# Optimization experiments

Hardware: AMD Instinct MI355X
Metric: run time of the kernel (lower is better)

Reference implementation:

```python
import jax, jax.numpy as jnp
import numpy as np

B, N, K = 8, 4096, 20
C_IN, H = 4, 64
EPS = 1e-5


def _bn(h, g, b):
    # BatchNorm1d in training mode: stats over all leading dims, per channel
    axes = tuple(range(h.ndim - 1))
    m = jnp.mean(h, axis=axes, keepdims=True)
    v = jnp.var(h, axis=axes, keepdims=True)
    return (h - m) * jax.lax.rsqrt(v + EPS) * g + b


def _edgeconv(x, k, w1, b1, g1, be1, w2, b2, g2, be2):
    # x: [B, N, C]. Dynamic kNN graph on current features (per cloud).
    x2 = jnp.sum(x * x, axis=-1)                       # [B, N]
    d = x2[:, :, None] + x2[:, None, :] - 2.0 * jnp.einsum('bnc,bmc->bnm', x, x)
    d = jax.lax.stop_gradient(d)                        # knn indices are non-differentiable
    _, idx = jax.lax.top_k(-d, k)                       # [B, N, k] nearest (incl. self)
    x_j = jax.vmap(lambda xb, ib: xb[ib])(x, idx)       # [B, N, k, C] gather
    x_i = jnp.broadcast_to(x[:, :, None, :], x_j.shape)
    msg = jnp.concatenate([x_i, x_j - x_i], axis=-1)    # [B, N, k, 2C]
    h = jax.nn.relu(_bn(msg @ w1 + b1, g1, be1))
    h = jax.nn.relu(_bn(h @ w2 + b2, g2, be2))
    return jnp.max(h, axis=2)                           # max aggregation over neighbors


def _forward(x,
             c1_w1, c1_b1, c1_g1, c1_be1, c1_w2, c1_b2, c1_g2, c1_be2,
             c2_w1, c2_b1, c2_g1, c2_be1, c2_w2, c2_b2, c2_g2, c2_be2,
             cls_w1, cls_b1, cls_g1, cls_be1, cls_w2, cls_b2):
    x1 = _edgeconv(x, K, c1_w1, c1_b1, c1_g1, c1_be1, c1_w2, c1_b2, c1_g2, c1_be2)   # [B,N,64]
    x2 = _edgeconv(x1, K, c2_w1, c2_b1, c2_g1, c2_be1, c2_w2, c2_b2, c2_g2, c2_be2)  # [B,N,128]
    xc = jnp.concatenate([x1, x2], axis=-1).reshape(B * N, 3 * H)                    # [BN,192]
    h = jax.nn.relu(_bn(xc @ cls_w1 + cls_b1, cls_g1, cls_be1))                      # dropout=identity (eval)
    return h @ cls_w2 + cls_b2                                                       # [BN, 1]


def setup_inputs() -> dict:
    key = jax.random.key(0)
    ks = iter(jax.random.split(key, 24))
    lin = lambda k, di, do: jax.random.normal(k, (di, do), jnp.float32) / np.sqrt(di)
    inp = {'x': jax.random.normal(next(ks), (B, N, C_IN), jnp.float32)}
    # conv1 nn: Linear(8,64)->BN->ReLU->Linear(64,64)->BN->ReLU
    inp.update(c1_w1=lin(next(ks), 2 * C_IN, H), c1_b1=jnp.zeros(H), c1_g1=jnp.ones(H), c1_be1=jnp.zeros(H),
               c1_w2=lin(next(ks), H, H), c1_b2=jnp.zeros(H), c1_g2=jnp.ones(H), c1_be2=jnp.zeros(H))
    # conv2 nn: Linear(128,128)->BN->ReLU->Linear(128,128)->BN->ReLU
    H2 = 2 * H
    inp.update(c2_w1=lin(next(ks), H2, H2), c2_b1=jnp.zeros(H2), c2_g1=jnp.ones(H2), c2_be1=jnp.zeros(H2),
               c2_w2=lin(next(ks), H2, H2), c2_b2=jnp.zeros(H2), c2_g2=jnp.ones(H2), c2_be2=jnp.zeros(H2))
    # classifier: Linear(192,128)->BN->ReLU->Dropout->Linear(128,1)
    inp.update(cls_w1=lin(next(ks), 3 * H, 128), cls_b1=jnp.zeros(128), cls_g1=jnp.ones(128), cls_be1=jnp.zeros(128),
               cls_w2=lin(next(ks), 128, 1), cls_b2=jnp.zeros(1))
    return inp


def reference(x,
              c1_w1, c1_b1, c1_g1, c1_be1, c1_w2, c1_b2, c1_g2, c1_be2,
              c2_w1, c2_b1, c2_g1, c2_be1, c2_w2, c2_b2, c2_g2, c2_be2,
              cls_w1, cls_b1, cls_g1, cls_be1, cls_w2, cls_b2):
    return _forward(x,
                    c1_w1, c1_b1, c1_g1, c1_be1, c1_w2, c1_b2, c1_g2, c1_be2,
                    c2_w1, c2_b1, c2_g1, c2_be1, c2_w2, c2_b2, c2_g2, c2_be2,
                    cls_w1, cls_b1, cls_g1, cls_be1, cls_w2, cls_b2)
```

## Files before the change

### kernel.cpp

```cpp
#include <hip/hip_runtime.h>
#include <math.h>

#define B_ 8
#define N_ 4096
#define K_ 20
#define KS_ 24
#define BN_ (B_*N_)

typedef __attribute__((ext_vector_type(8))) short bf16x8;
typedef __attribute__((ext_vector_type(4))) float f32x4;

__global__ __launch_bounds__(256) void finalize_parts_kernel(
    const double* __restrict__ part, int nb, int H, double invCount, float* __restrict__ st)
{
    __shared__ double red[256], red2[256];
    const int c = blockIdx.x, t = threadIdx.x;
    double s = 0., s2 = 0.;
    for (int b = t; b < nb; b += 256) {
        s  += part[(size_t)b*2*H + c];
        s2 += part[(size_t)b*2*H + H + c];
    }
    red[t] = s; red2[t] = s2;
    __syncthreads();
    #pragma unroll
    for (int off = 128; off; off >>= 1) {
        if (t < off) { red[t] += red[t+off]; red2[t] += red2[t+off]; }
        __syncthreads();
    }
    if (t == 0) {
        double mean = red[0] * invCount;
        double var  = fmax(red2[0] * invCount - mean * mean, 0.);
        st[2*H + c] = (float)mean;
        st[3*H + c] = (float)(1.0 / sqrt(var + 1e-5));
    }
}

__global__ __launch_bounds__(1024, 8) void knn4_kernel(const float* __restrict__ x, int* __restrict__ idxout)
{
    __shared__ float4 xt[N_];
    const int b = blockIdx.y;
    const int t = threadIdx.x;
    const float4* xg = (const float4*)x + b*N_;
    for (int e = t; e < N_; e += 1024) xt[e] = xg[e];
    __syncthreads();
    const int w = t >> 6, L = t & 63;
    const int n = blockIdx.x*16 + w;
    const float4 q = xt[n];
    const float MX = 3.4e38f;
    float m1 = MX, m2 = MX, m3 = MX; int i1 = 0, i2 = 0, i3 = 0;
    #pragma unroll 1
    for (int j = 0; j < 64; ++j) {
        float4 vv = xt[(j<<6) | L];
        float nn = vv.x*vv.x + vv.y*vv.y + vv.z*vv.z + vv.w*vv.w;
        float dp = q.x*vv.x + q.y*vv.y + q.z*vv.z + q.w*vv.w;
        float v = nn - 2.f*dp;
        bool c1 = v < m1, c2 = v < m2, c3 = v < m3;
        m3 = c2 ? m2 : (c3 ? v : m3);
        i3 = c2 ? i2 : (c3 ? j : i3);
        m2 = c1 ? m1 : (c2 ? v : m2);
        i2 = c1 ? i1 : (c2 ? j : i2);
        m1 = c1 ? v : m1;
        i1 = c1 ? j : i1;
    }
    unsigned long long used = 0;
    int mywin = 0;
    #pragma unroll 1
    for (int r = 0; r < K_; ++r) {
        float bv = m1; int bg = (i1<<6) | L;
        #pragma unroll
        for (int off = 32; off; off >>= 1) {
            float ov = __shfl_xor(bv, off);
            int   og = __shfl_xor(bg, off);
            bool tk = (ov < bv) || (ov == bv && og < bg);
            bv = tk ? ov : bv; bg = tk ? og : bg;
        }
        if (L == r) mywin = bg;
        if (L == (bg & 63)) {
            used |= 1ull << i1;
            m1 = m2; i1 = i2; m2 = m3; i2 = i3; m3 = MX;
            if (m1 == MX) {
                m2 = MX; m3 = MX; i1 = 0; i2 = 0; i3 = 0;
                #pragma unroll 1
                for (int j = 0; j < 64; ++j) {
                    float4 vv = xt[(j<<6) | L];
                    float nn = vv.x*vv.x + vv.y*vv.y + vv.z*vv.z + vv.w*vv.w;
                    float dp = q.x*vv.x + q.y*vv.y + q.z*vv.z + q.w*vv.w;
                    float dj = nn - 2.f*dp;
                    float v = ((used >> j) & 1ull) ? MX : dj;
                    bool c1 = v < m1, c2 = v < m2, c3 = v < m3;
                    m3 = c2 ? m2 : (c3 ? v : m3);
                    i3 = c2 ? i2 : (c3 ? j : i3);
                    m2 = c1 ? m1 : (c2 ? v : m2);
                    i2 = c1 ? i1 : (c2 ? j : i2);
                    m1 = c1 ? v : m1;
                    i1 = c1 ? j : i1;
                }
            }
        }
    }
    if (L < K_) idxout[(b*N_ + n)*K_ + L] = mywin;
}

static __device__ inline unsigned short f2bf(float f)
{
    unsigned u = __float_as_uint(f);
    unsigned r = (u + 0x7fffu + ((u >> 16) & 1u)) >> 16;
    return (unsigned short)r;
}

__global__ __launch_bounds__(256) void nrmprep_kernel(const float* __restrict__ x,
                                                      unsigned short* __restrict__ Xh,
                                                      unsigned short* __restrict__ Xl,
                                                      float* __restrict__ nrm)
{
    const int t = threadIdx.x, L = t & 63;
    const int row = blockIdx.x*4 + (t >> 6);
    const float v = x[row*64 + L];
    float s = v * v;
    #pragma unroll
    for (int off = 32; off; off >>= 1) s += __shfl_xor(s, off);
    if (L == 0) nrm[row] = s;
    unsigned short h = f2bf(v);
    float hf = __uint_as_float((unsigned)h << 16);
    unsigned short l = f2bf(v - hf);
    const size_t base = (size_t)(row >> 4)*1024 + (size_t)(L >> 3)*128 + (size_t)(row & 15)*8 + (size_t)(L & 7);
    Xh[base] = h;
    Xl[base] = l;
}

#define CE_(x,y) { float _t = fminf(x,y); y = fmaxf(x,y); x = _t; }
#define SORT8_(g0,g1,g2,g3,g4,g5,g6,g7)                                   \
    CE_(g0,g1) CE_(g2,g3) CE_(g4,g5) CE_(g6,g7)                           \
    CE_(g0,g2) CE_(g1,g3) CE_(g4,g6) CE_(g5,g7)                           \
    CE_(g1,g2) CE_(g5,g6)                                                 \
    CE_(g0,g4) CE_(g1,g5) CE_(g2,g6) CE_(g3,g7)                           \
    CE_(g2,g4) CE_(g3,g5)                                                 \
    CE_(g1,g2) CE_(g3,g4) CE_(g5,g6)
#define MERGE8_(g0,g1,g2,g3,g4,g5,g6,g7)                                  \
    sm0 = fminf(sm0,g7); sm1 = fminf(sm1,g6); sm2 = fminf(sm2,g5);        \
    sm3 = fminf(sm3,g4); sm4 = fminf(sm4,g3); sm5 = fminf(sm5,g2);        \
    sm6 = fminf(sm6,g1); sm7 = fminf(sm7,g0);                             \
    CE_(sm0,sm4) CE_(sm1,sm5) CE_(sm2,sm6) CE_(sm3,sm7)                   \
    CE_(sm0,sm2) CE_(sm1,sm3) CE_(sm4,sm6) CE_(sm5,sm7)                   \
    CE_(sm0,sm1) CE_(sm2,sm3) CE_(sm4,sm5) CE_(sm6,sm7)

__global__ __launch_bounds__(1024, 4) void knn64v4_kernel(
    const unsigned short* __restrict__ Xh, const unsigned short* __restrict__ Xl,
    const float* __restrict__ nrm, int* __restrict__ idx24)
{
    __shared__ float dist[16*512];
    const int b = blockIdx.y, t = threadIdx.x;
    const int w = t >> 6, L = t & 63;
    const int q0 = blockIdx.x * 16;
    const int m = L & 15, q4 = L >> 4;
    const size_t rowbase = (size_t)b * N_ * 64;
    const int swzW = q4 << 4;
    const int swzR = (w >> 2) << 4;
    const int fragoff = q4*128 + m*8;

    const unsigned short* aph = Xh + rowbase + (size_t)(q0 >> 4)*1024 + fragoff;
    const unsigned short* apl = Xl + rowbase + (size_t)(q0 >> 4)*1024 + fragoff;
    const bf16x8 a_h0 = *(const bf16x8*)(aph);
    const bf16x8 a_h1 = *(const bf16x8*)(aph + 512);
    const bf16x8 a_l0 = *(const bf16x8*)(apl);
    const bf16x8 a_l1 = *(const bf16x8*)(apl + 512);

    const float MX = 3.4e38f;
    float sm0 = MX, sm1 = MX, sm2 = MX, sm3 = MX, sm4 = MX, sm5 = MX, sm6 = MX, sm7 = MX;

    float* const wrow = dist + q4*2048;
    float* const rrow = dist + w*512 + (L ^ swzR);

    #pragma unroll 1
    for (int ck = 0; ck < 8; ++ck) {
        const unsigned slotW0 = (unsigned)(ck*8);
        const unsigned short* bp_h = Xh + rowbase + (size_t)(ck*32 + w*2)*1024 + fragoff;
        const unsigned short* bp_l = Xl + rowbase + (size_t)(ck*32 + w*2)*1024 + fragoff;
        const float* np = nrm + b*N_ + ck*512 + w*32 + m;
        int cm = w*32 + m;
        __syncthreads();
        #pragma unroll
        for (int tt = 0; tt < 2; ++tt) {
            bf16x8 b_h0 = *(const bf16x8*)(bp_h);
            bf16x8 b_h1 = *(const bf16x8*)(bp_h + 512);
            bf16x8 b_l0 = *(const bf16x8*)(bp_l);
            bf16x8 b_l1 = *(const bf16x8*)(bp_l + 512);
            f32x4 acc = {0.f, 0.f, 0.f, 0.f};
            acc = __builtin_amdgcn_mfma_f32_16x16x32_bf16(a_h0, b_h0, acc, 0, 0, 0);
            acc = __builtin_amdgcn_mfma_f32_16x16x32_bf16(a_h1, b_h1, acc, 0, 0, 0);
            acc = __builtin_amdgcn_mfma_f32_16x16x32_bf16(a_l0, b_h0, acc, 0, 0, 0);
            acc = __builtin_amdgcn_mfma_f32_16x16x32_bf16(a_l1, b_h1, acc, 0, 0, 0);
            acc = __builtin_amdgcn_mfma_f32_16x16x32_bf16(a_h0, b_l0, acc, 0, 0, 0);
            acc = __builtin_amdgcn_mfma_f32_16x16x32_bf16(a_h1, b_l1, acc, 0, 0, 0);
            const float nv = *np;
            const int colW = cm ^ swzW;
            const unsigned slotW = slotW0 + (unsigned)(cm >> 6);
            float* wp = wrow + colW;
            #pragma unroll
            for (int r = 0; r < 4; ++r) {
                float dv = nv - 2.f*acc[r];
                unsigned key = (__float_as_uint(dv) & ~63u) | slotW;
                wp[r*512] = __uint_as_float(key);
            }
            bp_h += 1024; bp_l += 1024; np += 16; cm += 16;
        }
        __syncthreads();
        {
            float g0 = rrow[0*64], g1 = rrow[1*64], g2 = rrow[2*64], g3 = rrow[3*64];
            float g4 = rrow[4*64], g5 = rrow[5*64], g6 = rrow[6*64], g7 = rrow[7*64];
            SORT8_(g0,g1,g2,g3,g4,g5,g6,g7)
            MERGE8_(g0,g1,g2,g3,g4,g5,g6,g7)
        }
    }

    int mywin = 0;
    #pragma unroll 1
    for (int sr = 0; sr < 3; ++sr) {
        float a0 = sm0, a1 = sm1, a2 = sm2, a3 = sm3, a4 = sm4, a5 = sm5, a6 = sm6, a7 = sm7;
        #pragma unroll
        for (int off = 32; off; off >>= 1) {
            float b0 = __shfl_xor(a0, off), b1 = __shfl_xor(a1, off);
            float b2 = __shfl_xor(a2, off), b3 = __shfl_xor(a3, off);
            float b4 = __shfl_xor(a4, off), b5 = __shfl_xor(a5, off);
            float b6 = __shfl_xor(a6, off), b7 = __shfl_xor(a7, off);
            float c0 = fminf(a0, b7), c1 = fminf(a1, b6), c2 = fminf(a2, b5), c3 = fminf(a3, b4);
            float c4 = fminf(a4, b3), c5 = fminf(a5, b2), c6 = fminf(a6, b1), c7 = fminf(a7, b0);
            float u;
            u = fminf(c0, c4); c4 = fmaxf(c0, c4); c0 = u;
            u = fminf(c1, c5); c5 = fmaxf(c1, c5); c1 = u;
            u = fminf(c2, c6); c6 = fmaxf(c2, c6); c2 = u;
            u = fminf(c3, c7); c7 = fmaxf(c3, c7); c3 = u;
            u = fminf(c0, c2); c2 = fmaxf(c0, c2); c0 = u;
            u = fminf(c1, c3); c3 = fmaxf(c1, c3); c1 = u;
            u = fminf(c4, c6); c6 = fmaxf(c4, c6); c4 = u;
            u = fminf(c5, c7); c7 = fmaxf(c5, c7); c5 = u;
            u = fminf(c0, c1); c1 = fmaxf(c0, c1); c0 = u;
            u = fminf(c2, c3); c3 = fmaxf(c2, c3); c2 = u;
            u = fminf(c4, c5); c5 = fmaxf(c4, c5); c4 = u;
            u = fminf(c6, c7); c7 = fmaxf(c6, c7); c6 = u;
            a0 = c0; a1 = c1; a2 = c2; a3 = c3; a4 = c4; a5 = c5; a6 = c6; a7 = c7;
        }
        #define POPW(AW, WIDX)                                                              \
        {                                                                                   \
            const unsigned long long bal = __ballot(sm0 == (AW));                           \
            const int owner = (int)__ffsll(bal) - 1;                                        \
            if (L == sr*8 + (WIDX))                                                         \
                mywin = (int)(((__float_as_uint(AW) & 63u) << 6) | (unsigned)owner);        \
            if (L == owner) {                                                               \
                sm0 = sm1; sm1 = sm2; sm2 = sm3; sm3 = sm4;                                 \
                sm4 = sm5; sm5 = sm6; sm6 = sm7; sm7 = MX;                                  \
            }                                                                               \
        }
        POPW(a0, 0) POPW(a1, 1) POPW(a2, 2) POPW(a3, 3)
        POPW(a4, 4) POPW(a5, 5) POPW(a6, 6) POPW(a7, 7)
        #undef POPW
    }
    if (L < KS_) idx24[((size_t)b*N_ + q0 + w)*KS_ + L] = mywin;
}

__global__ __launch_bounds__(256) void rescore_kernel(const float* __restrict__ x1, const float* __restrict__ nrm,
                                                      const int* __restrict__ idx24, int* __restrict__ idxout)
{
    const int t = threadIdx.x, w = t >> 6, L = t & 63;
    const int p = blockIdx.x*4 + w;
    const int bbase = p & ~(N_-1);
    const float MX = 3.4e38f;
    float dv = MX; int di = 0x7fffffff;
    if (L < KS_) {
        const int ci = idx24[(size_t)p*KS_ + L];
        const float4* qr = (const float4*)(x1 + (size_t)p*64);
        const float4* cr = (const float4*)(x1 + (size_t)(bbase + ci)*64);
        float dot = 0.f;
        #pragma unroll
        for (int i = 0; i < 16; ++i) {
            float4 a = qr[i], bx = cr[i];
            dot += a.x*bx.x + a.y*bx.y + a.z*bx.z + a.w*bx.w;
        }
        dv = __fsub_rn(__fadd_rn(nrm[p], nrm[bbase + ci]), 2.f*dot);
        di = ci;
    }
    int myfin = 0;
    #pragma unroll 1
    for (int r = 0; r < K_/2; ++r) {
        float v1 = dv; int g1 = di;
        float v2 = MX; int g2 = 0x7fffffff;
        #pragma unroll
        for (int off = 32; off; off >>= 1) {
            float ov1 = __shfl_xor(v1, off); int og1 = __shfl_xor(g1, off);
            float ov2 = __shfl_xor(v2, off); int og2 = __shfl_xor(g2, off);
            bool c1 = (ov1 < v1) || (ov1 == v1 && og1 < g1);
            float hv = c1 ? v1 : ov1; int hg = c1 ? g1 : og1;
            v1 = c1 ? ov1 : v1;       g1 = c1 ? og1 : g1;
            bool c2 = (ov2 < v2) || (ov2 == v2 && og2 < g2);
            float l2v = c2 ? ov2 : v2; int l2g = c2 ? og2 : g2;
            bool c3 = (l2v < hv) || (l2v == hv && l2g < hg);
            v2 = c3 ? l2v : hv;  g2 = c3 ? l2g : hg;
        }
        if (L == 2*r)   myfin = g1;
        if (L == 2*r+1) myfin = g2;
        if (di == g1 || di == g2) dv = MX;
    }
    if (L < K_) idxout[(size_t)p*K_ + L] = myfin;
}

__global__ __launch_bounds__(256) void pq1_kernel(const float* __restrict__ x, const float* __restrict__ W,
                                                  const float* __restrict__ b1,
                                                  float* __restrict__ P, float* __restrict__ Q)
{
    __shared__ float wd[256], wb[256];
    const int t = threadIdx.x;
    wd[t] = W[t] - W[256 + t];
    wb[t] = W[256 + t];
    __syncthreads();
    const int p = blockIdx.x*4 + (t >> 6), c = t & 63;
    const float4 xv = ((const float4*)x)[p];
    float Pv = b1[c] + xv.x*wd[c] + xv.y*wd[64+c] + xv.z*wd[128+c] + xv.w*wd[192+c];
    float Qv =         xv.x*wb[c] + xv.y*wb[64+c] + xv.z*wb[128+c] + xv.w*wb[192+c];
    P[p*64 + c] = Pv;
    Q[p*64 + c] = Qv;
}

__global__ __launch_bounds__(256) void pq2_kernel(const float* __restrict__ x1, const float* __restrict__ W,
                                                  const float* __restrict__ b1,
                                                  float* __restrict__ P, float* __restrict__ Q)
{
    __shared__ float wd[64*128], wb[64*128];
    const int t = threadIdx.x;
    for (int e = t; e < 8192; e += 256) {
        float wt = W[e], wbo = W[8192 + e];
        wd[e] = wt - wbo; wb[e] = wbo;
    }
    __syncthreads();
    const int pl = t >> 7, c = t & 127;
    const float b1v = b1[c];
    for (int p0 = blockIdx.x*2; p0 < BN_; p0 += gridDim.x*2) {
        const int p = p0 + pl;
        float Pv = b1v, Qv = 0.f;
        const float* xrow = x1 + p*64;
        #pragma unroll 8
        for (int k = 0; k < 64; ++k) {
            float xv = xrow[k];
            Pv += xv * wd[k*128 + c];
            Qv += xv * wb[k*128 + c];
        }
        P[p*128 + c] = Pv;
        Q[p*128 + c] = Qv;
    }
}

template<int HO>
__global__ __launch_bounds__(256) void stats_l1_kernel(const float* __restrict__ P, const float* __restrict__ Q,
                                                       const int* __restrict__ idx, double* __restrict__ partOut)
{
    constexpr int G = 256/HO;
    __shared__ double red[256], red2[256];
    const int t = threadIdx.x, c = t % HO, g = t / HO;
    double s = 0., s2 = 0.;
    for (int p = blockIdx.x; p < BN_; p += gridDim.x) {
        const float Pv = P[p*HO + c];
        const int bbase = p & ~(N_-1);
        for (int j = g; j < K_; j += G) {
            int m = idx[p*K_ + j];
            float z = Pv + Q[(bbase + m)*HO + c];
            double zd = (double)z;
            s += zd; s2 += zd*zd;
        }
    }
    red[t] = s; red2[t] = s2;
    __syncthreads();
    if (t < HO) {
        double a = red[t], a2 = red2[t];
        #pragma unroll
        for (int q = 1; q < G; ++q) { a += red[q*HO + t]; a2 += red2[q*HO + t]; }
        partOut[(size_t)blockIdx.x*(2*HO) + t] = a;
        partOut[(size_t)blockIdx.x*(2*HO) + HO + t] = a2;
    }
}

template<int HO>
__global__ __launch_bounds__(256) void conv_l2_kernel(
    const float* __restrict__ P, const float* __restrict__ Q, const int* __restrict__ idx,
    const float* __restrict__ st1, const float* __restrict__ g1, const float* __restrict__ be1,
    const float* __restrict__ w2, const float* __restrict__ b2,
    float* __restrict__ zmax, float* __restrict__ zmin, double* __restrict__ partOut)
{
    __shared__ float w2s[HO*64];
    __shared__ float h1s[K_*HO];
    __shared__ float redA[256], redB[256];
    __shared__ double redD[256], redD2[256];
    const int t = threadIdx.x;
    const int cy = blockIdx.y;
    for (int e = t; e < HO*64; e += 256) {
        int c = e >> 6, cl = e & 63;
        w2s[e] = w2[c*HO + cy*64 + cl];
    }
    const int cA = t % HO;
    const float mA = st1[2*HO + cA], rA = st1[3*HO + cA];
    const float gA = g1[cA], beA = be1[cA];
    const int c2l = t & 63, jh = t >> 6;
    const float b2v = b2[cy*64 + c2l];
    double ssum = 0., ssq = 0.;
    for (int p = blockIdx.x; p < BN_; p += gridDim.x) {
        __syncthreads();
        const int bbase = p & ~(N_-1);
        const float Pv = P[p*HO + cA];
        for (int e = t; e < K_*HO; e += 256) {
            int j = e / HO;
            int m = idx[p*K_ + j];
            float z = Pv + Q[(bbase + m)*HO + cA];
            float bn = __fadd_rn(__fmul_rn(__fmul_rn(__fsub_rn(z, mA), rA), gA), beA);
            h1s[e] = fmaxf(bn, 0.f);
        }
        __syncthreads();
        float acc[5];
        #pragma unroll
        for (int q = 0; q < 5; ++q) acc[q] = b2v;
        for (int c = 0; c < HO; ++c) {
            float wv = w2s[c*64 + c2l];
            #pragma unroll
            for (int q = 0; q < 5; ++q)
                acc[q] += h1s[(jh + q*4)*HO + c] * wv;
        }
        float mx = acc[0], mn = acc[0];
        #pragma unroll
        for (int q = 0; q < 5; ++q) {
            mx = fmaxf(mx, acc[q]); mn = fminf(mn, acc[q]);
            double ad = (double)acc[q];
            ssum += ad; ssq += ad*ad;
        }
        redA[t] = mx; redB[t] = mn;
        __syncthreads();
        if (t < 64) {
            float M = redA[t], Mn = redB[t];
            #pragma unroll
            for (int g = 1; g < 4; ++g) { M = fmaxf(M, redA[g*64 + t]); Mn = fminf(Mn, redB[g*64 + t]); }
            zmax[p*HO + cy*64 + t] = M;
            zmin[p*HO + cy*64 + t] = Mn;
        }
    }
    __syncthreads();
    redD[t] = ssum; redD2[t] = ssq;
    __syncthreads();
    if (t < 64) {
        double s = redD[t], s2 = redD2[t];
        #pragma unroll
        for (int g = 1; g < 4; ++g) { s += redD[g*64 + t]; s2 += redD2[g*64 + t]; }
        partOut[(size_t)blockIdx.x*(2*HO) + cy*64 + t] = s;
        partOut[(size_t)blockIdx.x*(2*HO) + HO + cy*64 + t] = s2;
    }
}

__global__ __launch_bounds__(256) void prep_w2t_kernel(const float* __restrict__ W,
                                                       unsigned short* __restrict__ wh,
                                                       unsigned short* __restrict__ wl, int HO)
{
    const int e = blockIdx.x*256 + threadIdx.x;
    const int k = e / HO, c = e % HO;
    const float v = W[e];
    unsigned short h = f2bf(v);
    float hf = __uint_as_float((unsigned)h << 16);
    wh[c*HO + k] = h;
    wl[c*HO + k] = f2bf(v - hf);
}

template<int HO>
__global__ __launch_bounds__(256) void conv_l2_mfma_kernel(
    const float* __restrict__ P, const float* __restrict__ Q, const int* __restrict__ idx,
    const float* __restrict__ st1, const float* __restrict__ g1, const float* __restrict__ be1,
    const unsigned short* __restrict__ w2h, const unsigned short* __restrict__ w2l,
    const float* __restrict__ b2,
    float* __restrict__ zmax, float* __restrict__ zmin, double* __restrict__ partOut)
{
    constexpr int HOP = HO + 8;
    constexpr int CDP = HO + 1;
    constexpr int CTW = HO / 64;
    constexpr int KSn = HO / 32;
    constexpr int HSH = (HO == 128) ? 7 : 6;
    __shared__ __align__(16) short hs[2*80*HOP];
    __shared__ int sidx[80];
    float* cd = (float*)hs;

    const int t = threadIdx.x, w = t >> 6, L = t & 63;
    const int m16 = L & 15, q4 = L >> 4;

    const int kT = t & (HO - 1);
    const float ac = st1[3*HO + kT] * g1[kT];
    const float bc = be1[kT] - st1[2*HO + kT] * ac;

    bf16x8 Bh[CTW][KSn], Bl[CTW][KSn];
    #pragma unroll
    for (int ctl = 0; ctl < CTW; ++ctl)
        #pragma unroll
        for (int ks = 0; ks < KSn; ++ks) {
            const int c  = w*16*CTW + ctl*16 + m16;
            const int k0 = ks*32 + q4*8;
            Bh[ctl][ks] = *(const bf16x8*)(w2h + c*HO + k0);
            Bl[ctl][ks] = *(const bf16x8*)(w2l + c*HO + k0);
        }

    const float b2c = (t < HO) ? b2[t] : 0.f;
    double ssum = 0., ssq = 0.;

    for (int p0 = blockIdx.x*4; p0 < BN_; p0 += gridDim.x*4) {
        const int bbase = p0 & ~(N_-1);
        __syncthreads();
        if (t < 80) sidx[t] = idx[p0*K_ + t];
        __syncthreads();
        for (int e = t; e < 80*HO; e += 256) {
            const int r  = e >> HSH;
            const int pl = (r*3277) >> 16;
            const int mI = sidx[r];
            float z = P[(size_t)(p0+pl)*HO + kT] + Q[(size_t)(bbase+mI)*HO + kT];
            float h = fmaxf(z*ac + bc, 0.f);
            unsigned short hh = f2bf(h);
            float hf = __uint_as_float((unsigned)hh << 16);
            unsigned short hl = f2bf(h - hf);
            hs[r*HOP + kT] = (short)hh;
            hs[80*HOP + r*HOP + kT] = (short)hl;
        }
        __syncthreads();
        f32x4 acc[5][CTW];
        #pragma unroll
        for (int rt = 0; rt < 5; ++rt)
            #pragma unroll
            for (int ctl = 0; ctl < CTW; ++ctl)
                acc[rt][ctl] = (f32x4){0.f, 0.f, 0.f, 0.f};
        #pragma unroll
        for (int rt = 0; rt < 5; ++rt)
            #pragma unroll
            for (int ks = 0; ks < KSn; ++ks) {
                const short* ap = hs + (rt*16 + m16)*HOP + ks*32 + q4*8;
                bf16x8 Ah = *(const bf16x8*)ap;
                bf16x8 Al = *(const bf16x8*)(ap + 80*HOP);
                #pragma unroll
                for (int ctl = 0; ctl < CTW; ++ctl) {
                    acc[rt][ctl] = __builtin_amdgcn_mfma_f32_16x16x32_bf16(Ah, Bh[ctl][ks], acc[rt][ctl], 0, 0, 0);
                    acc[rt][ctl] = __builtin_amdgcn_mfma_f32_16x16x32_bf16(Al, Bh[ctl][ks], acc[rt][ctl], 0, 0, 0);
                    acc[rt][ctl] = __builtin_amdgcn_mfma_f32_16x16x32_bf16(Ah, Bl[ctl][ks], acc[rt][ctl], 0, 0, 0);
                }
            }
        __syncthreads();
        #pragma unroll
        for (int rt = 0; rt < 5; ++rt)
            #pragma unroll
            for (int ctl = 0; ctl < CTW; ++ctl) {
                const int col = w*16*CTW + ctl*16 + m16;
                #pragma unroll
                for (int ri = 0; ri < 4; ++ri) {
                    const int row = rt*16 + q4*4 + ri;
                    cd[row*CDP + col] = acc[rt][ctl][ri];
                }
            }
        __syncthreads();
        if (t < HO) {
            #pragma unroll
            for (int pl = 0; pl < 4; ++pl) {
                float mx = -3.4e38f, mn = 3.4e38f;
                #pragma unroll
                for (int j = 0; j < K_; ++j) {
                    float v = cd[(pl*20 + j)*CDP + t] + b2c;
                    mx = fmaxf(mx, v); mn = fminf(mn, v);
                    double vd = (double)v;
                    ssum += vd; ssq += vd*vd;
                }
                zmax[(size_t)(p0+pl)*HO + t] = mx;
                zmin[(size_t)(p0+pl)*HO + t] = mn;
            }
        }
    }
    if (t < HO) {
        partOut[(size_t)blockIdx.x*(2*HO) + t] = ssum;
        partOut[(size_t)blockIdx.x*(2*HO) + HO + t] = ssq;
    }
}

template<int HO>
__global__ __launch_bounds__(256) void conv_fin_kernel(
    const float* __restrict__ zmax, const float* __restrict__ zmin,
    const float* __restrict__ st2, const float* __restrict__ g2, const float* __restrict__ be2,
    float* __restrict__ out)
{
    int e = blockIdx.x*256 + threadIdx.x;
    int c = e & (HO-1);
    float g = g2[c];
    float sel = (g >= 0.f) ? zmax[e] : zmin[e];
    float bn = __fadd_rn(__fmul_rn(__fmul_rn(__fsub_rn(sel, st2[2*HO + c]), st2[3*HO + c]), g), be2[c]);
    out[e] = fmaxf(bn, 0.f);
}

__global__ __launch_bounds__(256) void cls1_kernel(
    const float* __restrict__ x1, const float* __restrict__ x2f,
    const float* __restrict__ W, const float* __restrict__ b1,
    float* __restrict__ z, double* __restrict__ partOut)
{
    __shared__ float ws[192*64];
    __shared__ float xr[4*192];
    __shared__ double red[256], red2[256];
    const int t = threadIdx.x, cy = blockIdx.y;
    for (int e = t; e < 192*64; e += 256) {
        int c = e >> 6, cl = e & 63;
        ws[e] = W[c*128 + cy*64 + cl];
    }
    const int pl = t >> 6, c2l = t & 63;
    const float b1v = b1[cy*64 + c2l];
    double ssum = 0., ssq = 0.;
    for (int p0 = blockIdx.x*4; p0 < BN_; p0 += gridDim.x*4) {
        __syncthreads();
        for (int l = t; l < 4*192; l += 256) {
            int pp = l / 192, cc = l % 192;
            xr[l] = (cc < 64) ? x1[(p0+pp)*64 + cc] : x2f[(p0+pp)*128 + cc - 64];
        }
        __syncthreads();
        float acc = b1v;
        const float* xx = xr + pl*192;
        #pragma unroll 8
        for (int c = 0; c < 192; ++c) acc += xx[c] * ws[c*64 + c2l];
        z[(p0+pl)*128 + cy*64 + c2l] = acc;
        double ad = (double)acc;
        ssum += ad; ssq += ad*ad;
    }
    __syncthreads();
    red[t] = ssum; red2[t] = ssq;
    __syncthreads();
    if (t < 64) {
        double s = red[t], s2 = red2[t];
        #pragma unroll
        for (int g = 1; g < 4; ++g) { s += red[g*64 + t]; s2 += red2[g*64 + t]; }
        partOut[(size_t)blockIdx.x*256 + cy*64 + t] = s;
        partOut[(size_t)blockIdx.x*256 + 128 + cy*64 + t] = s2;
    }
}

__global__ __launch_bounds__(256) void cls_fin_kernel(
    const float* __restrict__ z, const float* __restrict__ st,
    const float* __restrict__ g, const float* __restrict__ be,
    const float* __restrict__ w2, const float* __restrict__ b2,
    float* __restrict__ out)
{
    const int t = threadIdx.x, w = t >> 6, L = t & 63;
    const int p = blockIdx.x*4 + w;
    float s = 0.f;
    #pragma unroll
    for (int h = 0; h < 2; ++h) {
        int c = L + h*64;
        float v = (z[p*128 + c] - st[256 + c]) * st[384 + c] * g[c] + be[c];
        s += fmaxf(v, 0.f) * w2[c];
    }
    #pragma unroll
    for (int off = 32; off; off >>= 1) s += __shfl_xor(s, off);
    if (L == 0) out[p] = s + b2[0];
}

extern "C" void kernel_launch(void* const* d_in, const int* in_sizes, int n_in,
                              void* d_out, int out_size, void* d_ws, size_t ws_size,
                              hipStream_t stream)
{
    const float* x      = (const float*)d_in[0];
    const float* c1_w1  = (const float*)d_in[1];
    const float* c1_b1  = (const float*)d_in[2];
    const float* c1_g1  = (const float*)d_in[3];
    const float* c1_be1 = (const float*)d_in[4];
    const float* c1_w2  = (const float*)d_in[5];
    const float* c1_b2  = (const float*)d_in[6];
    const float* c1_g2  = (const float*)d_in[7];
    const float* c1_be2 = (const float*)d_in[8];
    const float* c2_w1  = (const float*)d_in[9];
    const float* c2_b1  = (const float*)d_in[10];
    const float* c2_g1  = (const float*)d_in[11];
    const float* c2_be1 = (const float*)d_in[12];
    const float* c2_w2  = (const float*)d_in[13];
    const float* c2_b2  = (const float*)d_in[14];
    const float* c2_g2  = (const float*)d_in[15];
    const float* c2_be2 = (const float*)d_in[16];
    const float* cls_w1 = (const float*)d_in[17];
    const float* cls_b1 = (const float*)d_in[18];
    const float* cls_g1 = (const float*)d_in[19];
    const float* cls_be1= (const float*)d_in[20];
    const float* cls_w2 = (const float*)d_in[21];
    const float* cls_b2 = (const float*)d_in[22];
    (void)in_sizes; (void)n_in; (void)out_size; (void)ws_size;

    char* ws = (char*)d_ws;
    size_t off = 0;
    auto alloc = [&](size_t bytes) { char* p = ws + off; off += (bytes + 255) & ~255ull; return p; };
    float* A    = (float*)alloc((size_t)16<<20);
    float* Bq   = (float*)alloc((size_t)16<<20);
    float* zmax = (float*)alloc((size_t)16<<20);
    float* zmin = (float*)alloc((size_t)16<<20);
    float* x1b  = (float*)alloc((size_t)8<<20);
    float* x2b  = (float*)alloc((size_t)16<<20);
    int*   idx  = (int*)  alloc((size_t)BN_*K_*4);
    float* nrm  = (float*)alloc((size_t)BN_*4);
    float* st   = (float*)alloc((size_t)5*512*4);
    unsigned short* w2th = (unsigned short*)alloc((size_t)128*128*2);
    unsigned short* w2tl = (unsigned short*)alloc((size_t)128*128*2);
    float *st0 = st, *st1 = st+512, *st2 = st+1024, *st3 = st+1536, *st4 = st+2048;

    unsigned short* Xh = (unsigned short*)zmax;
    unsigned short* Xl = (unsigned short*)((char*)zmax + (4<<20));
    int* idx24 = (int*)x2b;
    double* part  = (double*)x2b;
    double* partC = (double*)Bq;

    knn4_kernel<<<dim3(N_/16, B_), 1024, 0, stream>>>(x, idx);
    pq1_kernel<<<BN_/4, 256, 0, stream>>>(x, c1_w1, c1_b1, A, Bq);
    stats_l1_kernel<64><<<2048, 256, 0, stream>>>(A, Bq, idx, part);
    finalize_parts_kernel<<<64, 256, 0, stream>>>(part, 2048, 64, 1.0/655360.0, st0);
    conv_l2_kernel<64><<<dim3(2048,1), 256, 0, stream>>>(A, Bq, idx, st0, c1_g1, c1_be1, c1_w2, c1_b2, zmax, zmin, part);
    finalize_parts_kernel<<<64, 256, 0, stream>>>(part, 2048, 64, 1.0/655360.0, st1);
    conv_fin_kernel<64><<<BN_*64/256, 256, 0, stream>>>(zmax, zmin, st1, c1_g2, c1_be2, x1b);

    nrmprep_kernel<<<BN_/4, 256, 0, stream>>>(x1b, Xh, Xl, nrm);
    knn64v4_kernel<<<dim3(N_/16, B_), 1024, 0, stream>>>(Xh, Xl, nrm, idx24);
    rescore_kernel<<<BN_/4, 256, 0, stream>>>(x1b, nrm, idx24, idx);
    pq2_kernel<<<1024, 256, 0, stream>>>(x1b, c2_w1, c2_b1, A, Bq);
    stats_l1_kernel<128><<<2048, 256, 0, stream>>>(A, Bq, idx, part);
    finalize_parts_kernel<<<128, 256, 0, stream>>>(part, 2048, 128, 1.0/655360.0, st2);
    prep_w2t_kernel<<<128*128/256, 256, 0, stream>>>(c2_w2, w2th, w2tl, 128);
    conv_l2_mfma_kernel<128><<<2048, 256, 0, stream>>>(A, Bq, idx, st2, c2_g1, c2_be1, w2th, w2tl, c2_b2, zmax, zmin, part);
    finalize_parts_kernel<<<128, 256, 0, stream>>>(part, 2048, 128, 1.0/655360.0, st3);
    conv_fin_kernel<128><<<BN_*128/256, 256, 0, stream>>>(zmax, zmin, st3, c2_g2, c2_be2, x2b);

    cls1_kernel<<<dim3(512,2), 256, 0, stream>>>(x1b, x2b, cls_w1, cls_b1, A, partC);
    finalize_parts_kernel<<<128, 256, 0, stream>>>(partC, 512, 128, 1.0/32768.0, st4);
    cls_fin_kernel<<<BN_/4, 256, 0, stream>>>(A, st4, cls_g1, cls_be1, cls_w2, cls_b2, (float*)d_out);
}
```

Before: 1.245 ms.

## Fuse layer-1 finalize with kNN prep and vectorize LDS reads

Merges conv_fin<64> and nrmprep into one kernel, so normalized layer-1 features are written and, in the same pass, converted to hi/lo bf16 tiles plus row norms. This drops one kernel launch and a re-read of x1. The split tiles now live in scratch space inside x2b, which has to stay clear of idx24 until the kNN kernel has consumed them. Separately, conv_l2 and cls1 now read shared-memory activations as float4, and cls1 loads its input rows with float4 global loads.

```diff
diff --git a/kernel.cpp b/kernel.cpp
--- a/kernel.cpp
+++ b/kernel.cpp
@@ -106,26 +106,6 @@
     unsigned u = __float_as_uint(f);
     unsigned r = (u + 0x7fffu + ((u >> 16) & 1u)) >> 16;
     return (unsigned short)r;
-}
-
-__global__ __launch_bounds__(256) void nrmprep_kernel(const float* __restrict__ x,
-                                                      unsigned short* __restrict__ Xh,
-                                                      unsigned short* __restrict__ Xl,
-                                                      float* __restrict__ nrm)
-{
-    const int t = threadIdx.x, L = t & 63;
-    const int row = blockIdx.x*4 + (t >> 6);
-    const float v = x[row*64 + L];
-    float s = v * v;
-    #pragma unroll
-    for (int off = 32; off; off >>= 1) s += __shfl_xor(s, off);
-    if (L == 0) nrm[row] = s;
-    unsigned short h = f2bf(v);
-    float hf = __uint_as_float((unsigned)h << 16);
-    unsigned short l = f2bf(v - hf);
-    const size_t base = (size_t)(row >> 4)*1024 + (size_t)(L >> 3)*128 + (size_t)(row & 15)*8 + (size_t)(L & 7);
-    Xh[base] = h;
-    Xl[base] = l;
 }
 
 #define CE_(x,y) { float _t = fminf(x,y); y = fmaxf(x,y); x = _t; }
@@ -385,7 +365,7 @@
     float* __restrict__ zmax, float* __restrict__ zmin, double* __restrict__ partOut)
 {
     __shared__ float w2s[HO*64];
-    __shared__ float h1s[K_*HO];
+    __shared__ __align__(16) float h1s[K_*HO];
     __shared__ float redA[256], redB[256];
     __shared__ double redD[256], redD2[256];
     const int t = threadIdx.x;
@@ -415,11 +395,20 @@
         float acc[5];
         #pragma unroll
         for (int q = 0; q < 5; ++q) acc[q] = b2v;
-        for (int c = 0; c < HO; ++c) {
-            float wv = w2s[c*64 + c2l];
+        const float4* h1v = (const float4*)h1s;
+        for (int c4 = 0; c4 < HO/4; ++c4) {
+            const float w0 = w2s[(c4*4+0)*64 + c2l];
+            const float w1 = w2s[(c4*4+1)*64 + c2l];
+            const float w2v = w2s[(c4*4+2)*64 + c2l];
+            const float w3 = w2s[(c4*4+3)*64 + c2l];
             #pragma unroll
-            for (int q = 0; q < 5; ++q)
-                acc[q] += h1s[(jh + q*4)*HO + c] * wv;
+            for (int q = 0; q < 5; ++q) {
+                float4 hv = h1v[(jh + q*4)*(HO/4) + c4];
+                acc[q] += hv.x*w0;
+                acc[q] += hv.y*w1;
+                acc[q] += hv.z*w2v;
+                acc[q] += hv.w*w3;
+            }
         }
         float mx = acc[0], mn = acc[0];
         #pragma unroll
@@ -588,13 +577,39 @@
     out[e] = fmaxf(bn, 0.f);
 }
 
+__global__ __launch_bounds__(256) void conv_fin64_prep_kernel(
+    const float* __restrict__ zmax, const float* __restrict__ zmin,
+    const float* __restrict__ st2, const float* __restrict__ g2, const float* __restrict__ be2,
+    float* __restrict__ out, unsigned short* __restrict__ Xh, unsigned short* __restrict__ Xl,
+    float* __restrict__ nrm)
+{
+    const int e = blockIdx.x*256 + threadIdx.x;
+    const int c = e & 63;
+    float g = g2[c];
+    float sel = (g >= 0.f) ? zmax[e] : zmin[e];
+    float bn = __fadd_rn(__fmul_rn(__fmul_rn(__fsub_rn(sel, st2[128 + c]), st2[192 + c]), g), be2[c]);
+    const float v = fmaxf(bn, 0.f);
+    out[e] = v;
+    float s = v * v;
+    #pragma unroll
+    for (int off = 32; off; off >>= 1) s += __shfl_xor(s, off);
+    const int row = e >> 6;
+    if (c == 0) nrm[row] = s;
+    unsigned short h = f2bf(v);
+    float hf = __uint_as_float((unsigned)h << 16);
+    unsigned short l = f2bf(v - hf);
+    const size_t base = (size_t)(row >> 4)*1024 + (size_t)(c >> 3)*128 + (size_t)(row & 15)*8 + (size_t)(c & 7);
+    Xh[base] = h;
+    Xl[base] = l;
+}
+
 __global__ __launch_bounds__(256) void cls1_kernel(
     const float* __restrict__ x1, const float* __restrict__ x2f,
     const float* __restrict__ W, const float* __restrict__ b1,
     float* __restrict__ z, double* __restrict__ partOut)
 {
     __shared__ float ws[192*64];
-    __shared__ float xr[4*192];
+    __shared__ __align__(16) float xr[4*192];
     __shared__ double red[256], red2[256];
     const int t = threadIdx.x, cy = blockIdx.y;
     for (int e = t; e < 192*64; e += 256) {
@@ -606,15 +621,23 @@
     double ssum = 0., ssq = 0.;
     for (int p0 = blockIdx.x*4; p0 < BN_; p0 += gridDim.x*4) {
         __syncthreads();
-        for (int l = t; l < 4*192; l += 256) {
-            int pp = l / 192, cc = l % 192;
-            xr[l] = (cc < 64) ? x1[(p0+pp)*64 + cc] : x2f[(p0+pp)*128 + cc - 64];
+        for (int l = t; l < 192; l += 256) {
+            int pp = l / 48, cc4 = l % 48;
+            float4 vsrc = (cc4 < 16)
+                ? ((const float4*)(x1 + (size_t)(p0+pp)*64))[cc4]
+                : ((const float4*)(x2f + (size_t)(p0+pp)*128))[cc4 - 16];
+            ((float4*)xr)[pp*48 + cc4] = vsrc;
         }
         __syncthreads();
         float acc = b1v;
-        const float* xx = xr + pl*192;
-        #pragma unroll 8
-        for (int c = 0; c < 192; ++c) acc += xx[c] * ws[c*64 + c2l];
+        const float4* xx4 = (const float4*)(xr + pl*192);
+        for (int c4 = 0; c4 < 48; ++c4) {
+            float4 hv = xx4[c4];
+            acc += hv.x * ws[(c4*4+0)*64 + c2l];
+            acc += hv.y * ws[(c4*4+1)*64 + c2l];
+            acc += hv.z * ws[(c4*4+2)*64 + c2l];
+            acc += hv.w * ws[(c4*4+3)*64 + c2l];
+        }
         z[(p0+pl)*128 + cy*64 + c2l] = acc;
         double ad = (double)acc;
         ssum += ad; ssq += ad*ad;
@@ -708,10 +731,13 @@
     finalize_parts_kernel<<<64, 256, 0, stream>>>(part, 2048, 64, 1.0/655360.0, st0);
     conv_l2_kernel<64><<<dim3(2048,1), 256, 0, stream>>>(A, Bq, idx, st0, c1_g1, c1_be1, c1_w2, c1_b2, zmax, zmin, part);
     finalize_parts_kernel<<<64, 256, 0, stream>>>(part, 2048, 64, 1.0/655360.0, st1);
-    conv_fin_kernel<64><<<BN_*64/256, 256, 0, stream>>>(zmax, zmin, st1, c1_g2, c1_be2, x1b);
-
-    nrmprep_kernel<<<BN_/4, 256, 0, stream>>>(x1b, Xh, Xl, nrm);
-    knn64v4_kernel<<<dim3(N_/16, B_), 1024, 0, stream>>>(Xh, Xl, nrm, idx24);
+    conv_fin64_prep_kernel<<<BN_*64/256, 256, 0, stream>>>(zmax, zmin, st1, c1_g2, c1_be2, x1b,
+                                                           (unsigned short*)((char*)x2b + (8<<20)),
+                                                           (unsigned short*)((char*)x2b + (12<<20)), nrm);
+    unsigned short* Xh2 = (unsigned short*)((char*)x2b + (8<<20));
+    unsigned short* Xl2 = (unsigned short*)((char*)x2b + (12<<20));
+
+    knn64v4_kernel<<<dim3(N_/16, B_), 1024, 0, stream>>>(Xh2, Xl2, nrm, idx24);
     rescore_kernel<<<BN_/4, 256, 0, stream>>>(x1b, nrm, idx24, idx);
     pq2_kernel<<<1024, 256, 0, stream>>>(x1b, c2_w1, c2_b1, A, Bq);
     stats_l1_kernel<128><<<2048, 256, 0, stream>>>(A, Bq, idx, part);
```

New measurement: 1.207 ms. 3.0% less time.
